# Performance work log

Hardware: AMD Instinct MI355X
Metric: run time of the kernel (lower is better)

## Reference

```python
import jax, jax.numpy as jnp
import numpy as np

TOP_K = 2

def setup_inputs() -> dict:
    key = jax.random.key(0)
    ks = jax.random.split(key, 5)
    B, T, D, F, E = 4, 2048, 1024, 4096, 8
    s = 0.02
    return {
        "x": jax.random.normal(ks[0], (B, T, D), jnp.float32),
        "gate_w": jax.random.normal(ks[1], (D, E), jnp.float32) * s,
        "w1": jax.random.normal(ks[2], (E, D, F), jnp.float32) * s,
        "w3": jax.random.normal(ks[3], (E, D, F), jnp.float32) * s,
        "w2": jax.random.normal(ks[4], (E, F, D), jnp.float32) * s,
    }

def reference(x, gate_w, w1, w3, w2):
    # Router: logits -> softmax -> top-k -> renormalize (eval mode: no jitter)
    logits = jnp.einsum("btd,de->bte", x, gate_w)          # (B,T,E)
    probs = jax.nn.softmax(logits, axis=-1)
    expert_weights, expert_indices = jax.lax.top_k(probs, TOP_K)  # (B,T,K)
    expert_weights = expert_weights / expert_weights.sum(-1, keepdims=True)

    E = w1.shape[0]
    out = jnp.zeros_like(x)
    # Loop over small fixed expert count; per-token weight is 0 for non-routed
    # tokens, so dense compute + weighted sum matches the masked gather/scatter.
    for i in range(E):
        wi = jnp.where(expert_indices == i, expert_weights, 0.0).sum(-1)  # (B,T)
        h = jax.nn.silu(jnp.einsum("btd,df->btf", x, w1[i])) \
            * jnp.einsum("btd,df->btf", x, w3[i])                         # SwiGLU
        out = out + jnp.einsum("btf,fd->btd", h, w2[i]) * wi[..., None]
    return out
```

## Files before the change

### kernel.cpp

```cpp
#include <hip/hip_runtime.h>
#include <hip/hip_bf16.h>


#define NTOK 8192
#define DMODEL 1024
#define FDIM 4096
#define NEXP 8

typedef __attribute__((ext_vector_type(8))) short s8v;
typedef __attribute__((ext_vector_type(4))) float f4v;

__device__ __forceinline__ int imin(int a, int b){ return a < b ? a : b; }

__device__ __forceinline__ unsigned short f2b(float f){
  union { float f; unsigned u; } v; v.f = f;
  unsigned r = v.u + 0x7fffu + ((v.u >> 16) & 1u);
  return (unsigned short)(r >> 16);
}

__device__ __forceinline__ f4v mfma16(s8v a, s8v b, f4v c){
  return __builtin_amdgcn_mfma_f32_16x16x32_bf16(a, b, c, 0, 0, 0);
}

#define GLDS16(gp, lp) __builtin_amdgcn_global_load_lds(                      \
    (const __attribute__((address_space(1))) void*)(gp),                      \
    (__attribute__((address_space(3))) void*)(lp), 16, 0, 0)


__global__ void k_cvt(const float4* __restrict__ in, ushort4* __restrict__ out, int n4){
  int i = blockIdx.x * blockDim.x + threadIdx.x;
  int st = gridDim.x * blockDim.x;
  for(; i < n4; i += st){
    float4 v = in[i];
    ushort4 o;
    o.x = f2b(v.x); o.y = f2b(v.y); o.z = f2b(v.z); o.w = f2b(v.w);
    out[i] = o;
  }
}

__global__ void k_tr(const float* __restrict__ in, unsigned short* __restrict__ out,
                     int R, int C){
  __shared__ float tile[32][33];
  const float* src = in + (size_t)blockIdx.z * R * C;
  unsigned short* dst = out + (size_t)blockIdx.z * R * C;
  int bx = blockIdx.x * 32, by = blockIdx.y * 32;
  int tx = threadIdx.x & 31, ty = threadIdx.x >> 5;
  #pragma unroll
  for(int i = 0; i < 32; i += 8)
    tile[ty + i][tx] = src[(size_t)(by + ty + i) * C + bx + tx];
  __syncthreads();
  #pragma unroll
  for(int i = 0; i < 32; i += 8)
    dst[(size_t)(bx + ty + i) * R + by + tx] = f2b(tile[tx][ty + i]);
}

__global__ void k_router(const float* __restrict__ x, const float* __restrict__ gw,
                         int* __restrict__ route_e, float* __restrict__ route_w,
                         int* __restrict__ counts){
  int lane = threadIdx.x & 63;
  int t = blockIdx.x * 4 + (threadIdx.x >> 6);
  const float* xr = x + (size_t)t * DMODEL;
  float acc[NEXP];
  #pragma unroll
  for(int e = 0; e < NEXP; e++) acc[e] = 0.f;
  for(int d = lane; d < DMODEL; d += 64){
    float xv = xr[d];
    const float* g = gw + d * NEXP;
    #pragma unroll
    for(int e = 0; e < NEXP; e++) acc[e] += xv * g[e];
  }
  #pragma unroll
  for(int off = 32; off > 0; off >>= 1){
    #pragma unroll
    for(int e = 0; e < NEXP; e++) acc[e] += __shfl_down(acc[e], off, 64);
  }
  if(lane == 0){
    float mx = acc[0];
    #pragma unroll
    for(int e = 1; e < NEXP; e++) mx = fmaxf(mx, acc[e]);
    float p[NEXP];
    #pragma unroll
    for(int e = 0; e < NEXP; e++) p[e] = expf(acc[e] - mx);
    int i0 = 0;
    #pragma unroll
    for(int e = 1; e < NEXP; e++) if(p[e] > p[i0]) i0 = e;
    int i1 = (i0 == 0) ? 1 : 0;
    #pragma unroll
    for(int e = 0; e < NEXP; e++) if(e != i0 && p[e] > p[i1]) i1 = e;
    float inv = 1.f / (p[i0] + p[i1]);
    route_e[2*t]   = i0; route_e[2*t+1] = i1;
    route_w[2*t]   = p[i0] * inv;
    route_w[2*t+1] = p[i1] * inv;
    atomicAdd(&counts[i0], 1); atomicAdd(&counts[i1], 1);
  }
}

__global__ void k_scan(const int* __restrict__ counts, int* __restrict__ offsets,
                       int* __restrict__ cursor){
  if(threadIdx.x == 0){
    int o = 0;
    for(int e = 0; e < NEXP; e++){ offsets[e] = o; o += counts[e]; cursor[e] = 0; }
    offsets[NEXP] = o;
  }
}

__global__ void k_fill(const int* __restrict__ route_e, const float* __restrict__ route_w,
                       const int* __restrict__ offsets, int* __restrict__ cursor,
                       int* __restrict__ pair_tok, float* __restrict__ pair_wt){
  int t = blockIdx.x * blockDim.x + threadIdx.x;
  if(t >= NTOK) return;
  #pragma unroll
  for(int k = 0; k < 2; k++){
    int e = route_e[2*t + k];
    int pos = atomicAdd(&cursor[e], 1);
    int gidx = offsets[e] + pos;
    pair_tok[gidx] = t;
    pair_wt[gidx] = route_w[2*t + k];
  }
}

__global__ __launch_bounds__(256, 2) void k_ffn1(
    const unsigned short* __restrict__ xb,
    const unsigned short* __restrict__ w1t,
    const unsigned short* __restrict__ w3t,
    const int* __restrict__ counts, const int* __restrict__ offsets,
    const int* __restrict__ pair_tok,
    unsigned short* __restrict__ h)
{
  int e = blockIdx.z;
  int cnt = counts[e];
  int m0 = blockIdx.x * 128;
  if(m0 >= cnt) return;
  int off = offsets[e];
  int n0 = blockIdx.y * 128;

  __shared__ short As[128*32];
  __shared__ short B1s[128*32];
  __shared__ short B3s[128*32];
  __shared__ int stok[128];

  int tid = threadIdx.x;
  if(tid < 128){
    int pr = m0 + tid;
    stok[tid] = pair_tok[off + imin(pr, cnt - 1)];
  }
  __syncthreads();

  int wave = tid >> 6, lane = tid & 63;
  int rr  = wave * 32 + (lane >> 2);
  int g16 = (((lane & 3) ^ ((lane >> 3) & 3))) * 16;

  const char* a0 = (const char*)xb + (size_t)stok[rr]      * (DMODEL*2) + g16;
  const char* a1 = (const char*)xb + (size_t)stok[rr + 16] * (DMODEL*2) + g16;
  const char* b1base = (const char*)w1t + ((size_t)e * FDIM + n0) * (DMODEL*2);
  const char* b3base = (const char*)w3t + ((size_t)e * FDIM + n0) * (DMODEL*2);
  const char* b1_0 = b1base + (size_t)rr * (DMODEL*2) + g16;
  const char* b1_1 = b1_0 + (size_t)16 * (DMODEL*2);
  const char* b3_0 = b3base + (size_t)rr * (DMODEL*2) + g16;
  const char* b3_1 = b3_0 + (size_t)16 * (DMODEL*2);

  short* adst0  = As  + wave*32*32;  short* adst1  = adst0  + 16*32;
  short* b1dst0 = B1s + wave*32*32;  short* b1dst1 = b1dst0 + 16*32;
  short* b3dst0 = B3s + wave*32*32;  short* b3dst1 = b3dst0 + 16*32;

  f4v zero = {0.f, 0.f, 0.f, 0.f};
  f4v acc1[4][4], acc3[4][4];
  #pragma unroll
  for(int i = 0; i < 4; i++)
    #pragma unroll
    for(int j = 0; j < 4; j++){ acc1[i][j] = zero; acc3[i][j] = zero; }

  int wm = wave & 1, wn = wave >> 1;
  int lm = lane & 15, quad = lane >> 4;
  int rp = (quad ^ ((lm >> 1) & 3)) * 8;

  for(int kt = 0; kt < DMODEL; kt += 32){
    int kb = kt * 2;
    __syncthreads();
    GLDS16(a0  + kb, adst0);  GLDS16(a1  + kb, adst1);
    GLDS16(b1_0 + kb, b1dst0); GLDS16(b1_1 + kb, b1dst1);
    GLDS16(b3_0 + kb, b3dst0); GLDS16(b3_1 + kb, b3dst1);
    __syncthreads();

    s8v af[4], b1f[4], b3f[4];
    #pragma unroll
    for(int mi = 0; mi < 4; mi++)
      af[mi] = *(const s8v*)(As + (wm*64 + mi*16 + lm)*32 + rp);
    #pragma unroll
    for(int ni = 0; ni < 4; ni++){
      b1f[ni] = *(const s8v*)(B1s + (wn*64 + ni*16 + lm)*32 + rp);
      b3f[ni] = *(const s8v*)(B3s + (wn*64 + ni*16 + lm)*32 + rp);
    }
    #pragma unroll
    for(int mi = 0; mi < 4; mi++)
      #pragma unroll
      for(int ni = 0; ni < 4; ni++){
        acc1[mi][ni] = mfma16(af[mi], b1f[ni], acc1[mi][ni]);
        acc3[mi][ni] = mfma16(af[mi], b3f[ni], acc3[mi][ni]);
      }
  }

  #pragma unroll
  for(int mi = 0; mi < 4; mi++){
    int prb = m0 + wm*64 + mi*16 + quad*4;
    #pragma unroll
    for(int i = 0; i < 4; i++){
      int pr = prb + i;
      if(pr < cnt){
        size_t hrow = (size_t)(off + pr) * FDIM + n0 + wn*64 + lm;
        #pragma unroll
        for(int ni = 0; ni < 4; ni++){
          float p = acc1[mi][ni][i];
          float q = acc3[mi][ni][i];
          float hv = (p / (1.f + __expf(-p))) * q;
          h[hrow + ni*16] = f2b(hv);
        }
      }
    }
  }
}

__global__ __launch_bounds__(256, 2) void k_ffn2(
    const unsigned short* __restrict__ h,
    const unsigned short* __restrict__ w2t,
    const int* __restrict__ counts, const int* __restrict__ offsets,
    const int* __restrict__ pair_tok, const float* __restrict__ pair_wt,
    float* __restrict__ out)
{
  int e = blockIdx.z;
  int cnt = counts[e];
  int m0 = blockIdx.x * 128;
  if(m0 >= cnt) return;
  int off = offsets[e];
  int n0 = blockIdx.y * 128;

  __shared__ short As[128*32];
  __shared__ short Bs[128*32];

  int tid = threadIdx.x, wave = tid >> 6, lane = tid & 63;
  int rr  = wave * 32 + (lane >> 2);
  int g16 = (((lane & 3) ^ ((lane >> 3) & 3))) * 16;

  int pr0 = imin(m0 + rr,      cnt - 1);
  int pr1 = imin(m0 + rr + 16, cnt - 1);
  const char* a0 = (const char*)h + (size_t)(off + pr0) * (FDIM*2) + g16;
  const char* a1 = (const char*)h + (size_t)(off + pr1) * (FDIM*2) + g16;
  const char* bbase = (const char*)w2t + ((size_t)e * DMODEL + n0) * (FDIM*2);
  const char* b0 = bbase + (size_t)rr * (FDIM*2) + g16;
  const char* b1p = b0 + (size_t)16 * (FDIM*2);

  short* adst0 = As + wave*32*32;  short* adst1 = adst0 + 16*32;
  short* bdst0 = Bs + wave*32*32;  short* bdst1 = bdst0 + 16*32;

  f4v zero = {0.f, 0.f, 0.f, 0.f};
  f4v acc[4][4];
  #pragma unroll
  for(int i = 0; i < 4; i++)
    #pragma unroll
    for(int j = 0; j < 4; j++) acc[i][j] = zero;

  int wm = wave & 1, wn = wave >> 1;
  int lm = lane & 15, quad = lane >> 4;
  int rp = (quad ^ ((lm >> 1) & 3)) * 8;

  for(int kt = 0; kt < FDIM; kt += 32){
    int kb = kt * 2;
    __syncthreads();
    GLDS16(a0 + kb, adst0);  GLDS16(a1 + kb, adst1);
    GLDS16(b0 + kb, bdst0);  GLDS16(b1p + kb, bdst1);
    __syncthreads();

    s8v af[4], bf[4];
    #pragma unroll
    for(int mi = 0; mi < 4; mi++)
      af[mi] = *(const s8v*)(As + (wm*64 + mi*16 + lm)*32 + rp);
    #pragma unroll
    for(int ni = 0; ni < 4; ni++)
      bf[ni] = *(const s8v*)(Bs + (wn*64 + ni*16 + lm)*32 + rp);
    #pragma unroll
    for(int mi = 0; mi < 4; mi++)
      #pragma unroll
      for(int ni = 0; ni < 4; ni++)
        acc[mi][ni] = mfma16(af[mi], bf[ni], acc[mi][ni]);
  }

  #pragma unroll
  for(int mi = 0; mi < 4; mi++){
    int prb = m0 + wm*64 + mi*16 + quad*4;
    #pragma unroll
    for(int i = 0; i < 4; i++){
      int pr = prb + i;
      if(pr < cnt){
        int gp = off + pr;
        int tok = pair_tok[gp];
        float wt = pair_wt[gp];
        float* orow = out + (size_t)tok * DMODEL + n0 + wn*64 + lm;
        #pragma unroll
        for(int ni = 0; ni < 4; ni++)
          atomicAdd(orow + ni*16, acc[mi][ni][i] * wt);
      }
    }
  }
}

extern "C" void kernel_launch(void* const* d_in, const int* in_sizes, int n_in,
                              void* d_out, int out_size, void* d_ws, size_t ws_size,
                              hipStream_t stream){
  const float* x  = (const float*)d_in[0];
  const float* gw = (const float*)d_in[1];
  const float* w1 = (const float*)d_in[2];
  const float* w3 = (const float*)d_in[3];
  const float* w2 = (const float*)d_in[4];
  float* out = (float*)d_out;

  char* ws = (char*)d_ws;
  size_t o = 0;
  auto alloc = [&](size_t b){ size_t r = o; o += (b + 255) & ~(size_t)255; return r; };
  unsigned short* xb  = (unsigned short*)(ws + alloc((size_t)NTOK * DMODEL * 2));
  unsigned short* w1t = (unsigned short*)(ws + alloc((size_t)NEXP * DMODEL * FDIM * 2));
  unsigned short* w3t = (unsigned short*)(ws + alloc((size_t)NEXP * DMODEL * FDIM * 2));
  unsigned short* w2t = (unsigned short*)(ws + alloc((size_t)NEXP * DMODEL * FDIM * 2));
  unsigned short* h   = (unsigned short*)(ws + alloc((size_t)2 * NTOK * FDIM * 2));
  int*   route_e  = (int*)  (ws + alloc(2 * NTOK * 4));
  float* route_w  = (float*)(ws + alloc(2 * NTOK * 4));
  int*   counts   = (int*)  (ws + alloc(256));
  int*   offsets  = (int*)  (ws + alloc(256));
  int*   cursor   = (int*)  (ws + alloc(256));
  int*   pair_tok = (int*)  (ws + alloc(2 * NTOK * 4));
  float* pair_wt  = (float*)(ws + alloc(2 * NTOK * 4));

  hipMemsetAsync(counts, 0, 256, stream);
  hipMemsetAsync(out, 0, (size_t)out_size * 4, stream);

  k_cvt<<<2048, 256, 0, stream>>>((const float4*)x, (ushort4*)xb, NTOK * DMODEL / 4);
  k_tr<<<dim3(FDIM/32, DMODEL/32, NEXP), 256, 0, stream>>>(w1, w1t, DMODEL, FDIM);
  k_tr<<<dim3(FDIM/32, DMODEL/32, NEXP), 256, 0, stream>>>(w3, w3t, DMODEL, FDIM);
  k_tr<<<dim3(DMODEL/32, FDIM/32, NEXP), 256, 0, stream>>>(w2, w2t, FDIM, DMODEL);

  k_router<<<NTOK/4, 256, 0, stream>>>(x, gw, route_e, route_w, counts);
  k_scan<<<1, 64, 0, stream>>>(counts, offsets, cursor);
  k_fill<<<NTOK/256, 256, 0, stream>>>(route_e, route_w, offsets, cursor, pair_tok, pair_wt);

  k_ffn1<<<dim3(64, FDIM/128, NEXP), 256, 0, stream>>>(xb, w1t, w3t, counts, offsets, pair_tok, h);
  k_ffn2<<<dim3(64, DMODEL/128, NEXP), 256, 0, stream>>>(h, w2t, counts, offsets, pair_tok, pair_wt, out);
}
```

Baseline: 1.621 ms.

## Double-buffer LDS tiles in expert GEMMs and replace atomic scatter with combine kernel

Both FFN kernels now double-buffer their LDS tiles: the global-to-LDS loads for the next K step are issued before the MFMAs on the current buffer, with one barrier per iteration instead of two. The second GEMM also stops scattering with float atomicAdd into the output. It writes weighted per-pair rows into a buffer that reuses the w1t workspace, and a new combine kernel sums each token's two pair rows, so the output memset goes away. This doubles LDS use, which may cut occupancy, and adds an extra pass over the per-pair output buffer.

New measurement: 1.630 ms. No clear change (+0.6%).

```diff
diff --git a/kernel.cpp b/kernel.cpp
--- a/kernel.cpp
+++ b/kernel.cpp
@@ -106,7 +106,8 @@
 
 __global__ void k_fill(const int* __restrict__ route_e, const float* __restrict__ route_w,
                        const int* __restrict__ offsets, int* __restrict__ cursor,
-                       int* __restrict__ pair_tok, float* __restrict__ pair_wt){
+                       int* __restrict__ pair_tok, float* __restrict__ pair_wt,
+                       int* __restrict__ t2p){
   int t = blockIdx.x * blockDim.x + threadIdx.x;
   if(t >= NTOK) return;
   #pragma unroll
@@ -116,6 +117,7 @@
     int gidx = offsets[e] + pos;
     pair_tok[gidx] = t;
     pair_wt[gidx] = route_w[2*t + k];
+    t2p[2*t + k] = gidx;
   }
 }
 
@@ -134,9 +136,9 @@
   int off = offsets[e];
   int n0 = blockIdx.y * 128;
 
-  __shared__ short As[128*32];
-  __shared__ short B1s[128*32];
-  __shared__ short B3s[128*32];
+  __shared__ short As[2][128*32];
+  __shared__ short B1s[2][128*32];
+  __shared__ short B3s[2][128*32];
   __shared__ int stok[128];
 
   int tid = threadIdx.x;
@@ -149,6 +151,7 @@
   int wave = tid >> 6, lane = tid & 63;
   int rr  = wave * 32 + (lane >> 2);
   int g16 = (((lane & 3) ^ ((lane >> 3) & 3))) * 16;
+  int wo = wave * 32 * 32;
 
   const char* a0 = (const char*)xb + (size_t)stok[rr]      * (DMODEL*2) + g16;
   const char* a1 = (const char*)xb + (size_t)stok[rr + 16] * (DMODEL*2) + g16;
@@ -159,10 +162,6 @@
   const char* b3_0 = b3base + (size_t)rr * (DMODEL*2) + g16;
   const char* b3_1 = b3_0 + (size_t)16 * (DMODEL*2);
 
-  short* adst0  = As  + wave*32*32;  short* adst1  = adst0  + 16*32;
-  short* b1dst0 = B1s + wave*32*32;  short* b1dst1 = b1dst0 + 16*32;
-  short* b3dst0 = B3s + wave*32*32;  short* b3dst1 = b3dst0 + 16*32;
-
   f4v zero = {0.f, 0.f, 0.f, 0.f};
   f4v acc1[4][4], acc3[4][4];
   #pragma unroll
@@ -174,22 +173,34 @@
   int lm = lane & 15, quad = lane >> 4;
   int rp = (quad ^ ((lm >> 1) & 3)) * 8;
 
+  GLDS16(a0,   As[0]  + wo); GLDS16(a1,   As[0]  + wo + 512);
+  GLDS16(b1_0, B1s[0] + wo); GLDS16(b1_1, B1s[0] + wo + 512);
+  GLDS16(b3_0, B3s[0] + wo); GLDS16(b3_1, B3s[0] + wo + 512);
+  __syncthreads();
+
   for(int kt = 0; kt < DMODEL; kt += 32){
-    int kb = kt * 2;
-    __syncthreads();
-    GLDS16(a0  + kb, adst0);  GLDS16(a1  + kb, adst1);
-    GLDS16(b1_0 + kb, b1dst0); GLDS16(b1_1 + kb, b1dst1);
-    GLDS16(b3_0 + kb, b3dst0); GLDS16(b3_1 + kb, b3dst1);
-    __syncthreads();
-
+    int c = (kt >> 5) & 1;
+    if(kt + 32 < DMODEL){
+      int kb = (kt + 32) * 2;
+      short* an  = As[c^1]  + wo;
+      short* b1n = B1s[c^1] + wo;
+      short* b3n = B3s[c^1] + wo;
+      GLDS16(a0   + kb, an);  GLDS16(a1   + kb, an  + 512);
+      GLDS16(b1_0 + kb, b1n); GLDS16(b1_1 + kb, b1n + 512);
+      GLDS16(b3_0 + kb, b3n); GLDS16(b3_1 + kb, b3n + 512);
+    }
+
+    const short* Ab  = As[c];
+    const short* B1b = B1s[c];
+    const short* B3b = B3s[c];
     s8v af[4], b1f[4], b3f[4];
     #pragma unroll
     for(int mi = 0; mi < 4; mi++)
-      af[mi] = *(const s8v*)(As + (wm*64 + mi*16 + lm)*32 + rp);
+      af[mi] = *(const s8v*)(Ab + (wm*64 + mi*16 + lm)*32 + rp);
     #pragma unroll
     for(int ni = 0; ni < 4; ni++){
-      b1f[ni] = *(const s8v*)(B1s + (wn*64 + ni*16 + lm)*32 + rp);
-      b3f[ni] = *(const s8v*)(B3s + (wn*64 + ni*16 + lm)*32 + rp);
+      b1f[ni] = *(const s8v*)(B1b + (wn*64 + ni*16 + lm)*32 + rp);
+      b3f[ni] = *(const s8v*)(B3b + (wn*64 + ni*16 + lm)*32 + rp);
     }
     #pragma unroll
     for(int mi = 0; mi < 4; mi++)
@@ -198,6 +209,7 @@
         acc1[mi][ni] = mfma16(af[mi], b1f[ni], acc1[mi][ni]);
         acc3[mi][ni] = mfma16(af[mi], b3f[ni], acc3[mi][ni]);
       }
+    __syncthreads();
   }
 
   #pragma unroll
@@ -224,8 +236,8 @@
     const unsigned short* __restrict__ h,
     const unsigned short* __restrict__ w2t,
     const int* __restrict__ counts, const int* __restrict__ offsets,
-    const int* __restrict__ pair_tok, const float* __restrict__ pair_wt,
-    float* __restrict__ out)
+    const float* __restrict__ pair_wt,
+    float* __restrict__ pout)
 {
   int e = blockIdx.z;
   int cnt = counts[e];
@@ -234,12 +246,13 @@
   int off = offsets[e];
   int n0 = blockIdx.y * 128;
 
-  __shared__ short As[128*32];
-  __shared__ short Bs[128*32];
+  __shared__ short As[2][128*32];
+  __shared__ short Bs[2][128*32];
 
   int tid = threadIdx.x, wave = tid >> 6, lane = tid & 63;
   int rr  = wave * 32 + (lane >> 2);
   int g16 = (((lane & 3) ^ ((lane >> 3) & 3))) * 16;
+  int wo = wave * 32 * 32;
 
   int pr0 = imin(m0 + rr,      cnt - 1);
   int pr1 = imin(m0 + rr + 16, cnt - 1);
@@ -249,9 +262,6 @@
   const char* b0 = bbase + (size_t)rr * (FDIM*2) + g16;
   const char* b1p = b0 + (size_t)16 * (FDIM*2);
 
-  short* adst0 = As + wave*32*32;  short* adst1 = adst0 + 16*32;
-  short* bdst0 = Bs + wave*32*32;  short* bdst1 = bdst0 + 16*32;
-
   f4v zero = {0.f, 0.f, 0.f, 0.f};
   f4v acc[4][4];
   #pragma unroll
@@ -263,25 +273,35 @@
   int lm = lane & 15, quad = lane >> 4;
   int rp = (quad ^ ((lm >> 1) & 3)) * 8;
 
+  GLDS16(a0, As[0] + wo); GLDS16(a1,  As[0] + wo + 512);
+  GLDS16(b0, Bs[0] + wo); GLDS16(b1p, Bs[0] + wo + 512);
+  __syncthreads();
+
   for(int kt = 0; kt < FDIM; kt += 32){
-    int kb = kt * 2;
-    __syncthreads();
-    GLDS16(a0 + kb, adst0);  GLDS16(a1 + kb, adst1);
-    GLDS16(b0 + kb, bdst0);  GLDS16(b1p + kb, bdst1);
-    __syncthreads();
-
+    int c = (kt >> 5) & 1;
+    if(kt + 32 < FDIM){
+      int kb = (kt + 32) * 2;
+      short* an = As[c^1] + wo;
+      short* bn = Bs[c^1] + wo;
+      GLDS16(a0  + kb, an); GLDS16(a1  + kb, an + 512);
+      GLDS16(b0  + kb, bn); GLDS16(b1p + kb, bn + 512);
+    }
+
+    const short* Ab = As[c];
+    const short* Bb = Bs[c];
     s8v af[4], bf[4];
     #pragma unroll
     for(int mi = 0; mi < 4; mi++)
-      af[mi] = *(const s8v*)(As + (wm*64 + mi*16 + lm)*32 + rp);
+      af[mi] = *(const s8v*)(Ab + (wm*64 + mi*16 + lm)*32 + rp);
     #pragma unroll
     for(int ni = 0; ni < 4; ni++)
-      bf[ni] = *(const s8v*)(Bs + (wn*64 + ni*16 + lm)*32 + rp);
+      bf[ni] = *(const s8v*)(Bb + (wn*64 + ni*16 + lm)*32 + rp);
     #pragma unroll
     for(int mi = 0; mi < 4; mi++)
       #pragma unroll
       for(int ni = 0; ni < 4; ni++)
         acc[mi][ni] = mfma16(af[mi], bf[ni], acc[mi][ni]);
+    __syncthreads();
   }
 
   #pragma unroll
@@ -292,15 +312,22 @@
       int pr = prb + i;
       if(pr < cnt){
         int gp = off + pr;
-        int tok = pair_tok[gp];
         float wt = pair_wt[gp];
-        float* orow = out + (size_t)tok * DMODEL + n0 + wn*64 + lm;
+        float* prow = pout + (size_t)gp * DMODEL + n0 + wn*64 + lm;
         #pragma unroll
         for(int ni = 0; ni < 4; ni++)
-          atomicAdd(orow + ni*16, acc[mi][ni][i] * wt);
+          prow[ni*16] = acc[mi][ni][i] * wt;
       }
     }
   }
+}
+
+__global__ void k_combine(const float4* __restrict__ pout, const int* __restrict__ t2p,
+                          float4* __restrict__ out){
+  int t = blockIdx.x;
+  int d = threadIdx.x;
+  int p0 = t2p[2*t], p1 = t2p[2*t + 1];
+  out[(size_t)t * 256 + d] = pout[(size_t)p0 * 256 + d] + pout[(size_t)p1 * 256 + d];
 }
 
 extern "C" void kernel_launch(void* const* d_in, const int* in_sizes, int n_in,
@@ -328,9 +355,10 @@
   int*   cursor   = (int*)  (ws + alloc(256));
   int*   pair_tok = (int*)  (ws + alloc(2 * NTOK * 4));
   float* pair_wt  = (float*)(ws + alloc(2 * NTOK * 4));
+  int*   t2p      = (int*)  (ws + alloc(2 * NTOK * 4));
+  float* pout = (float*)w1t;
 
   hipMemsetAsync(counts, 0, 256, stream);
-  hipMemsetAsync(out, 0, (size_t)out_size * 4, stream);
 
   k_cvt<<<2048, 256, 0, stream>>>((const float4*)x, (ushort4*)xb, NTOK * DMODEL / 4);
   k_tr<<<dim3(FDIM/32, DMODEL/32, NEXP), 256, 0, stream>>>(w1, w1t, DMODEL, FDIM);
@@ -339,8 +367,9 @@
 
   k_router<<<NTOK/4, 256, 0, stream>>>(x, gw, route_e, route_w, counts);
   k_scan<<<1, 64, 0, stream>>>(counts, offsets, cursor);
-  k_fill<<<NTOK/256, 256, 0, stream>>>(route_e, route_w, offsets, cursor, pair_tok, pair_wt);
+  k_fill<<<NTOK/256, 256, 0, stream>>>(route_e, route_w, offsets, cursor, pair_tok, pair_wt, t2p);
 
   k_ffn1<<<dim3(64, FDIM/128, NEXP), 256, 0, stream>>>(xb, w1t, w3t, counts, offsets, pair_tok, h);
-  k_ffn2<<<dim3(64, DMODEL/128, NEXP), 256, 0, stream>>>(h, w2t, counts, offsets, pair_tok, pair_wt, out);
-}
+  k_ffn2<<<dim3(64, DMODEL/128, NEXP), 256, 0, stream>>>(h, w2t, counts, offsets, pair_wt, pout);
+  k_combine<<<NTOK, 256, 0, stream>>>((const float4*)pout, t2p, (float4*)out);
+}
```
